# Kernel optimization log

Hardware: AMD Instinct MI355X
Metric: run time of the kernel (lower is better)

## Reference

```python
import jax, jax.numpy as jnp
import numpy as np

B, T, K, H = 8, 1024, 128, 8
TOP_K = 64
KS = 5  # conv kernel size for Q/K
DN = ('NCH', 'OIH', 'NCH')


def setup_inputs() -> dict:
    key = jax.random.key(0)
    ks = jax.random.split(key, 9)
    s = 0.05
    return {
        'x': jax.random.normal(ks[0], (B, T, K), jnp.float32),
        'Wq': jax.random.normal(ks[1], (K * H, K, KS), jnp.float32) * s,
        'bq': jax.random.normal(ks[2], (K * H,), jnp.float32) * s,
        'Wk': jax.random.normal(ks[3], (K * H, K, KS), jnp.float32) * s,
        'bk': jax.random.normal(ks[4], (K * H,), jnp.float32) * s,
        'Wv': jax.random.normal(ks[5], (K * H, K, 1), jnp.float32) * s,
        'bv': jax.random.normal(ks[6], (K * H,), jnp.float32) * s,
        'Wu': jax.random.normal(ks[7], (K, K * H), jnp.float32) * s,
        'bu': jax.random.normal(ks[8], (K,), jnp.float32) * s,
    }


def _prep(z, b, k, h, t, scale):
    # z: (b, k*h, t) conv output; torch view(b,k,h,t) then transposes -> (b,h,t,k)
    z = z.reshape(b, k, h, t)
    z = jnp.transpose(z, (0, 2, 3, 1)) * scale  # (b, h, t, k)
    # torch: transpose(1,2).contiguous().view(b*h, t, k) -- replicate exactly
    z = jnp.transpose(z, (0, 2, 1, 3)).reshape(b * h, t, k)
    return z


def reference(x, Wq, bq, Wk, bk, Wv, bv, Wu, bu):
    b, t, k = x.shape
    h = H
    xc = jnp.transpose(x, (0, 2, 1))  # (b, k, t)
    # causal left-pad KS-1 for Q/K convs; V is pointwise (kernel 1)
    q = jax.lax.conv_general_dilated(xc, Wq, (1,), [(KS - 1, 0)], dimension_numbers=DN) + bq[None, :, None]
    kk = jax.lax.conv_general_dilated(xc, Wk, (1,), [(KS - 1, 0)], dimension_numbers=DN) + bk[None, :, None]
    v = jax.lax.conv_general_dilated(xc, Wv, (1,), [(0, 0)], dimension_numbers=DN) + bv[None, :, None]
    scale = k ** -0.25
    q = _prep(q, b, k, h, t, scale)
    kk = _prep(kk, b, k, h, t, scale)
    v = _prep(v, b, k, h, t, 1.0)
    w = jnp.einsum('btk,bsk->bts', q, kk)  # (b*h, t, t)
    # top-k sparsification: keep entries >= k-th largest per row, else row min
    largest, _ = jax.lax.top_k(w, TOP_K)
    thresh = jnp.min(largest, axis=-1, keepdims=True)
    row_min = jnp.min(w, axis=-1, keepdims=True)
    w = jnp.where(w >= thresh, w, row_min)
    # causal mask (strict upper triangle -> -inf)
    causal = jnp.triu(jnp.ones((t, t), bool), 1)
    w = jnp.where(causal[None], -jnp.inf, w)
    w = jax.nn.softmax(w, axis=-1)
    out = jnp.einsum('bts,bsk->btk', w, v)  # (b*h, t, k)
    out = out.reshape(b, h, t, k)
    out = jnp.transpose(out, (0, 2, 1, 3)).reshape(b, t, k * h)
    return out @ Wu.T + bu
```

## Files before the change

kernel.cpp:

```cpp
#include <hip/hip_runtime.h>
#include <hip/hip_fp16.h>
#include <cstdint>

using f16 = _Float16;
typedef __attribute__((ext_vector_type(8))) _Float16 f16x8;
typedef __attribute__((ext_vector_type(4))) _Float16 f16x4;
typedef __attribute__((ext_vector_type(4))) float f32x4;

#define MFMA16(a, b, c) __builtin_amdgcn_mfma_f32_16x16x32_f16((a), (b), (c), 0, 0, 0)

__device__ __forceinline__ f16x8 ldfrag(const f16* p) { return *(const f16x8*)p; }

__device__ __forceinline__ void dma16(const f16* g, f16* l) {
  __builtin_amdgcn_global_load_lds(
      (const __attribute__((address_space(1))) void*)g,
      (__attribute__((address_space(3))) void*)l, 16, 0, 0);
}
__device__ __forceinline__ void wait_vm0() {
  asm volatile("s_waitcnt vmcnt(0)" ::: "memory");
}
__device__ __forceinline__ void wait_lgkm0() {
  asm volatile("s_waitcnt lgkmcnt(0)" ::: "memory");
}
__device__ __forceinline__ void wait_vm4() {
  asm volatile("s_waitcnt vmcnt(4)" ::: "memory");
}
__device__ __forceinline__ void wait_vm2() {
  asm volatile("s_waitcnt vmcnt(2)" ::: "memory");
}

static const int64_t NX = 1048576;
static const int64_t NW = 655360;
static const int64_t NV = 131072;

__global__ __launch_bounds__(256) void k0_prep(
    const float* __restrict__ x, const float* __restrict__ Wq,
    const float* __restrict__ Wk, const float* __restrict__ Wv,
    const float* __restrict__ Wu,
    f16* __restrict__ xh, f16* __restrict__ xl,
    f16* __restrict__ Wqh, f16* __restrict__ Wql,
    f16* __restrict__ Wkh, f16* __restrict__ Wkl,
    f16* __restrict__ Wvb, f16* __restrict__ Wub) {
  int64_t i = (int64_t)blockIdx.x * 256 + threadIdx.x;
  if (i < NX) {
    const float v = x[i];
    const f16 h = (f16)v;
    xh[i] = h; xl[i] = (f16)(v - (float)h);
  } else if (i < NX + NW) {
    int64_t d = i - NX;
    int j = (int)(d >> 17);
    int rem = (int)(d & 131071);
    int o = rem >> 7, c = rem & 127;
    const float v = Wq[(int64_t)(o * 128 + c) * 5 + j];
    const f16 h = (f16)v;
    Wqh[d] = h; Wql[d] = (f16)(v - (float)h);
  } else if (i < NX + 2 * NW) {
    int64_t d = i - NX - NW;
    int j = (int)(d >> 17);
    int rem = (int)(d & 131071);
    int o = rem >> 7, c = rem & 127;
    const float v = Wk[(int64_t)(o * 128 + c) * 5 + j];
    const f16 h = (f16)v;
    Wkh[d] = h; Wkl[d] = (f16)(v - (float)h);
  } else if (i < NX + 2 * NW + NV) {
    int64_t d = i - NX - 2 * NW;
    Wvb[d] = (f16)Wv[d];
  } else {
    int64_t d = i - NX - 2 * NW - NV;
    Wub[d] = (f16)Wu[d];
  }
}

#define STAGE_QK(DST, PASS, VALEXPR)                                    \
  {                                                                     \
    __syncthreads();                                                    \
    _Pragma("unroll")                                                   \
    for (int nt = 0; nt < 8; ++nt) {                                    \
      const int o = o0 + nt * 16 + lo;                                  \
      const int kcl = (o >> 3) & 63, hh = o & 7;                        \
      _Pragma("unroll")                                                 \
      for (int rtl = 0; rtl < 2; ++rtl) {                               \
        const int rt = (PASS) * 2 + rtl;                                \
        _Pragma("unroll")                                               \
        for (int r = 0; r < 4; ++r) {                                   \
          const int t2l = (rtl * 16 + quad * 4 + r) * 8 + hh;           \
          lds[t2l * 72 + kcl] = (VALEXPR);                              \
        }                                                               \
      }                                                                 \
    }                                                                   \
    __syncthreads();                                                    \
    _Pragma("unroll")                                                   \
    for (int p = 0; p < 8; ++p) {                                       \
      const int idx = p * 256 + tid;                                    \
      const int a = idx >> 3, c8 = (idx & 7) * 8;                       \
      *(f16x8*)(DST + ((int64_t)m * 1024 + t2b + (PASS) * 256 + a) * 128 + \
                half * 64 + c8) = *(const f16x8*)&lds[a * 72 + c8];     \
    }                                                                   \
  }

__global__ __launch_bounds__(256) void k1_conv(
    const f16* __restrict__ xh, const f16* __restrict__ xl,
    const f16* __restrict__ Wqh, const f16* __restrict__ Wql,
    const f16* __restrict__ Wkh, const f16* __restrict__ Wkl,
    const f16* __restrict__ Wvb,
    const float* __restrict__ bq, const float* __restrict__ bk,
    const float* __restrict__ bv,
    f16* __restrict__ q3h, f16* __restrict__ q3l,
    f16* __restrict__ k3h, f16* __restrict__ k3l,
    f16* __restrict__ v3T) {
  __shared__ f16 shm[36384];
  f16* const wbuf = shm;
  f16* const xbuf = shm + 18432;
  f16* const lds  = shm;
  const int tid = threadIdx.x;
  const int w = tid >> 6, lane = tid & 63;
  const int quad = lane >> 4, lo = lane & 15;
  const int r0 = blockIdx.x * 64;
  const int bb = r0 >> 10;
  const int m  = r0 >> 7;
  const int t2b = (r0 & 127) * 8;
  const int tloc = r0 & 1023;
  const int half = blockIdx.y;
  const int isK = blockIdx.z;
  const int o0 = half * 512 + w * 128;

  const f16* Wh = isK ? Wkh : Wqh;
  const f16* Wl = isK ? Wkl : Wql;
  const float* bias = isK ? bk : bq;

#pragma unroll
  for (int p = 0; p < 9; ++p) {
    const int u = p * 256 + tid;
    if (u < 2176) {
      const int row = u >> 5, tz = (u >> 4) & 1, c8 = (u & 15) * 8;
      int lt = tloc - 4 + row;
      if (lt < 0) lt = 0;
      const f16* src = (tz ? xl : xh) + ((int64_t)(bb * 1024 + lt)) * 128 + c8;
      *(f16x8*)&xbuf[row * 264 + tz * 128 + c8] = *(const f16x8*)src;
    }
  }
  __syncthreads();

  const int64_t wlane = (int64_t)(lane & 15) * 128 + (lane >> 4) * 8;

  if (!isK) {
    f32x4 av[4][8];
#pragma unroll
    for (int rt = 0; rt < 4; ++rt)
#pragma unroll
      for (int i = 0; i < 8; ++i)
#pragma unroll
        for (int r = 0; r < 4; ++r) av[rt][i][r] = 0.f;

#pragma unroll
    for (int g = 0; g < 4; ++g) {
#pragma unroll
      for (int s = 0; s < 2; ++s) {
        const int64_t vsrc = (int64_t)(o0 + (g * 2 + s) * 16) * 128 + wlane;
#pragma unroll
        for (int kk = 0; kk < 4; ++kk)
          dma16(Wvb + vsrc + kk * 32, wbuf + w * 4096 + s * 2048 + kk * 512);
      }
      wait_vm0();
#pragma unroll
      for (int kk = 0; kk < 4; ++kk) {
        f16x8 a[4];
#pragma unroll
        for (int rt = 0; rt < 4; ++rt)
          a[rt] = *(const f16x8*)&xbuf[(rt * 16 + lo + 4) * 264 + kk * 32 +
                                       quad * 8];
#pragma unroll
        for (int s = 0; s < 2; ++s) {
          const f16x8 bv8 = *(const f16x8*)&wbuf[w * 4096 + s * 2048 + kk * 512 +
                                                 quad * 128 + lo * 8];
#pragma unroll
          for (int rt = 0; rt < 4; ++rt)
            av[rt][g * 2 + s] = MFMA16(a[rt], bv8, av[rt][g * 2 + s]);
        }
      }
      wait_lgkm0();
    }
    __syncthreads();
#pragma unroll
    for (int pass = 0; pass < 2; ++pass) {
#pragma unroll
      for (int nt = 0; nt < 8; ++nt) {
        const int o = o0 + nt * 16 + lo;
        const float vbv = bv[o];
        const int kcl = (o >> 3) & 63, hh = o & 7;
#pragma unroll
        for (int rtl = 0; rtl < 2; ++rtl)
#pragma unroll
          for (int r = 0; r < 4; ++r) {
            const int t2l = (rtl * 16 + quad * 4 + r) * 8 + hh;
            lds[kcl * 264 + t2l] = (f16)(av[pass * 2 + rtl][nt][r] + vbv);
          }
      }
      __syncthreads();
#pragma unroll
      for (int p = 0; p < 8; ++p) {
        const int idx = p * 256 + tid;
        const int kcl = idx >> 5, t8 = (idx & 31) * 8;
        *(f16x8*)(v3T + ((int64_t)m * 128 + half * 64 + kcl) * 1024 + t2b +
                  pass * 256 + t8) = *(const f16x8*)&lds[kcl * 264 + t8];
      }
      __syncthreads();
    }
  }

  f32x4 aq[4][8];
#pragma unroll
  for (int rt = 0; rt < 4; ++rt)
#pragma unroll
    for (int i = 0; i < 8; ++i)
#pragma unroll
      for (int r = 0; r < 4; ++r) { aq[rt][i][r] = 0.f; }

  const int64_t wbase = wlane + (int64_t)o0 * 128;
#define ISSUE_HALF(J, KK, NTG, H)                                       \
  {                                                                     \
    _Pragma("unroll")                                                   \
    for (int ntl2 = 0; ntl2 < 2; ++ntl2) {                              \
      const int ntl_ = (H) * 2 + ntl2;                                  \
      const int64_t o_ = wbase + (int64_t)(J) * 131072 + (KK) * 32 +    \
                         (int64_t)(((NTG) * 4 + ntl_) * 16) * 128;      \
      dma16(Wh + o_, wbuf + w * 4096 + ntl_ * 1024);                    \
      dma16(Wl + o_, wbuf + w * 4096 + ntl_ * 1024 + 512);              \
    }                                                                   \
  }

  ISSUE_HALF(0, 0, 0, 0)
  ISSUE_HALF(0, 0, 0, 1)

  const bool z0 = (tloc == 0);
  for (int j = 0; j < 5; ++j) {
    f16x8 ah[4], al[4];
#pragma unroll
    for (int c = 0; c < 8; ++c) {
      const int kk = c >> 1, ntg = c & 1;
      if (ntg == 0) {
#pragma unroll
        for (int rt = 0; rt < 4; ++rt) {
          ah[rt] = *(const f16x8*)&xbuf[(rt * 16 + lo + j) * 264 + kk * 32 +
                                        quad * 8];
          al[rt] = *(const f16x8*)&xbuf[(rt * 16 + lo + j) * 264 + 128 +
                                        kk * 32 + quad * 8];
        }
        if (z0 && (lo + j < 4)) {
#pragma unroll
          for (int e = 0; e < 8; ++e) { ah[0][e] = (f16)0; al[0][e] = (f16)0; }
        }
      }
      const int nj = (c == 7) ? j + 1 : j;
      const int nkk = (c == 7) ? 0 : ((c + 1) >> 1);
      const int nntg = (c == 7) ? 0 : ((c + 1) & 1);
      const bool more = (c < 7) || (j < 4);

      wait_vm4();
#pragma unroll
      for (int ntl = 0; ntl < 2; ++ntl) {
        const int nt = ntg * 4 + ntl;
        const f16x8 bh = *(const f16x8*)&wbuf[w * 4096 + ntl * 1024 +
                                              quad * 128 + lo * 8];
        const f16x8 bl = *(const f16x8*)&wbuf[w * 4096 + ntl * 1024 + 512 +
                                              quad * 128 + lo * 8];
#pragma unroll
        for (int rt = 0; rt < 4; ++rt) {
          aq[rt][nt] = MFMA16(ah[rt], bh, aq[rt][nt]);
          aq[rt][nt] = MFMA16(ah[rt], bl, aq[rt][nt]);
          aq[rt][nt] = MFMA16(al[rt], bh, aq[rt][nt]);
        }
      }
      wait_lgkm0();
      if (more) ISSUE_HALF(nj, nkk, nntg, 0)

      if (c == 7) {
        if (j == 4) wait_vm0(); else wait_vm4();
      } else {
        wait_vm4();
      }
#pragma unroll
      for (int ntl = 2; ntl < 4; ++ntl) {
        const int nt = ntg * 4 + ntl;
        const f16x8 bh = *(const f16x8*)&wbuf[w * 4096 + ntl * 1024 +
                                              quad * 128 + lo * 8];
        const f16x8 bl = *(const f16x8*)&wbuf[w * 4096 + ntl * 1024 + 512 +
                                              quad * 128 + lo * 8];
#pragma unroll
        for (int rt = 0; rt < 4; ++rt) {
          aq[rt][nt] = MFMA16(ah[rt], bh, aq[rt][nt]);
          aq[rt][nt] = MFMA16(ah[rt], bl, aq[rt][nt]);
          aq[rt][nt] = MFMA16(al[rt], bh, aq[rt][nt]);
        }
      }
      wait_lgkm0();
      if (more) ISSUE_HALF(nj, nkk, nntg, 1)
    }
  }
#undef ISSUE_HALF

  const float SC = 0.29730177875068026f;
#pragma unroll
  for (int nt = 0; nt < 8; ++nt) {
    const int o = o0 + nt * 16 + lo;
    const float vb = bias[o];
#pragma unroll
    for (int rt = 0; rt < 4; ++rt)
#pragma unroll
      for (int r = 0; r < 4; ++r) aq[rt][nt][r] = (aq[rt][nt][r] + vb) * SC;
  }

  if (!isK) {
    STAGE_QK(q3h, 0, (f16)aq[rt][nt][r])
    STAGE_QK(q3h, 1, (f16)aq[rt][nt][r])
    STAGE_QK(q3l, 0, (f16)(aq[rt][nt][r] - (float)(f16)aq[rt][nt][r]))
    STAGE_QK(q3l, 1, (f16)(aq[rt][nt][r] - (float)(f16)aq[rt][nt][r]))
  } else {
    STAGE_QK(k3h, 0, (f16)aq[rt][nt][r])
    STAGE_QK(k3h, 1, (f16)aq[rt][nt][r])
    STAGE_QK(k3l, 0, (f16)(aq[rt][nt][r] - (float)(f16)aq[rt][nt][r]))
    STAGE_QK(k3l, 1, (f16)(aq[rt][nt][r] - (float)(f16)aq[rt][nt][r]))
  }
}

__global__ __launch_bounds__(512, 4) void k234_attn(
    const f16* __restrict__ q3h, const f16* __restrict__ q3l,
    const f16* __restrict__ k3h, const f16* __restrict__ k3l,
    const f16* __restrict__ v3T, f16* __restrict__ A) {
  __shared__ __align__(16) char smem[70144];
  float* const SbQ = (float*)smem;
  f16* const PbufA = (f16*)smem;
  f16* const PbufB = (f16*)(smem + 16640);
  f16* const kbuf = (f16*)(smem + 33280);
  f16* const qlds = (f16*)(smem + 66048);
  const int tid = threadIdx.x;
  const int w = tid >> 6, lane = tid & 63;
  const int quad = lane >> 4, lo = lane & 15;
  const int qd = lane & 3, cit = lane >> 2;
  const int qsw = qd ^ ((cit >> 1) & 3);
  const int fro = (lo * 4 + (quad ^ ((lo >> 1) & 3))) * 8;
  const int hid = blockIdx.y * 32 + blockIdx.x;
  const int m = (hid & 7) * 8 + ((hid >> 3) >> 5);
  const int r0 = ((hid >> 3) & 31) * 32;

  unsigned key[2][2][16];
  unsigned kmn[2][2];
#pragma unroll
  for (int g = 0; g < 2; ++g)
#pragma unroll
    for (int rr = 0; rr < 2; ++rr) kmn[g][rr] = 0xFFFFFFFFu;

#pragma unroll
  for (int half = 0; half < 2; ++half) {
    f32x4 acc[2][4];
#pragma unroll
    for (int g = 0; g < 2; ++g)
#pragma unroll
      for (int i = 0; i < 4; ++i)
#pragma unroll
        for (int r = 0; r < 4; ++r) acc[g][i][r] = 0.f;

    for (int kp = 0; kp < 2; ++kp) {
#pragma unroll
      for (int kkh = 0; kkh < 2; ++kkh) {
        __syncthreads();
        if (w < 4) {
          const int h_ = w & 1, grp_ = w >> 1;
          const f16* qsrc = (h_ ? q3l : q3h) +
              ((int64_t)m * 1024 + r0 + grp_ * 16 + lo) * 128 +
              (kp * 2 + kkh) * 32 + quad * 8;
          dma16(qsrc, qlds + w * 512);
        }
        wait_vm0();
        __syncthreads();

#define KISS(CC, PAIR)                                                   \
  {                                                                      \
    const int64_t rowg =                                                 \
        (int64_t)(m * 1024 + half * 512 + (CC) * 128 + w * 16 + cit) *   \
            128 + (kp * 2 + kkh) * 32 + qsw * 8;                         \
    dma16(k3h + rowg, kbuf + (w * 4 + (PAIR) * 2) * 512);                \
    dma16(k3l + rowg, kbuf + (w * 4 + (PAIR) * 2 + 1) * 512);            \
  }
        KISS(0, 0)
        KISS(1, 1)
#pragma unroll
        for (int cc = 0; cc < 4; ++cc) {
          if (cc < 3) wait_vm2();
          else wait_vm0();
          const int pair = cc & 1;
          const f16x8 qh0 = ldfrag(qlds + 0 * 512 + lane * 8);
          const f16x8 ql0 = ldfrag(qlds + 1 * 512 + lane * 8);
          const f16x8 qh1 = ldfrag(qlds + 2 * 512 + lane * 8);
          const f16x8 ql1 = ldfrag(qlds + 3 * 512 + lane * 8);
          const f16x8 bh =
              *(const f16x8*)(kbuf + (w * 4 + pair * 2) * 512 + fro);
          const f16x8 bl =
              *(const f16x8*)(kbuf + (w * 4 + pair * 2 + 1) * 512 + fro);
          acc[0][cc] = MFMA16(qh0, bh, acc[0][cc]);
          acc[0][cc] = MFMA16(qh0, bl, acc[0][cc]);
          acc[0][cc] = MFMA16(ql0, bh, acc[0][cc]);
          acc[1][cc] = MFMA16(qh1, bh, acc[1][cc]);
          acc[1][cc] = MFMA16(qh1, bl, acc[1][cc]);
          acc[1][cc] = MFMA16(ql1, bh, acc[1][cc]);
          wait_lgkm0();
          if (cc == 0) KISS(2, 0)
          if (cc == 1) KISS(3, 1)
        }
#undef KISS
      }
    }

#pragma unroll
    for (int grp = 0; grp < 2; ++grp) {
#pragma unroll
      for (int q = 0; q < 2; ++q) {
#pragma unroll
        for (int c2 = 0; c2 < 2; ++c2)
#pragma unroll
          for (int r = 0; r < 4; ++r)
            SbQ[(quad * 4 + r) * 268 + c2 * 128 + w * 16 + lo] =
                acc[grp][q * 2 + c2][r];
        __syncthreads();
#pragma unroll
        for (int rr = 0; rr < 2; ++rr) {
          const float4 f4 =
              *(const float4*)(SbQ + (w * 2 + rr) * 268 + lane * 4);
          const float fe[4] = {f4.x, f4.y, f4.z, f4.w};
#pragma unroll
          for (int e = 0; e < 4; ++e) {
            const unsigned u = __builtin_bit_cast(unsigned, fe[e]);
            const unsigned k = (u & 0x80000000u) ? ~u : (u | 0x80000000u);
            key[grp][rr][half * 8 + q * 4 + e] = k;
            kmn[grp][rr] = min(kmn[grp][rr], k);
          }
        }
        __syncthreads();
      }
    }
  }

  const int64_t vrow = (int64_t)(m * 128 + w * 16 + cit) * 1024;
  const int nkbM = ((r0 + 16) >> 6) + 1;
#define VISSUE(KB, PAIR)                                                 \
  {                                                                      \
    dma16(v3T + vrow + (KB) * 64 + qsw * 8,                              \
          kbuf + (w * 4 + (PAIR) * 2) * 512);                            \
    dma16(v3T + vrow + (KB) * 64 + 32 + qsw * 8,                         \
          kbuf + (w * 4 + (PAIR) * 2 + 1) * 512);                       \
  }
  VISSUE(0, 0)
  if (nkbM > 1) VISSUE(1, 1)

#pragma unroll
  for (int off = 32; off; off >>= 1) {
#pragma unroll
    for (int g = 0; g < 2; ++g)
#pragma unroll
      for (int rr = 0; rr < 2; ++rr)
        kmn[g][rr] = min(kmn[g][rr],
                         (unsigned)__shfl_xor((int)kmn[g][rr], off));
  }
  unsigned th[2][2] = {{0u, 0u}, {0u, 0u}};
  {
    bool dn[2][2] = {{false, false}, {false, false}};
    for (int b = 31; b >= 0; --b) {
      bool all = true;
#pragma unroll
      for (int g = 0; g < 2; ++g)
#pragma unroll
        for (int rr = 0; rr < 2; ++rr) {
          if (!dn[g][rr]) {
            const unsigned c = th[g][rr] | (1u << b);
            int cnt = 0;
#pragma unroll
            for (int i = 0; i < 16; ++i)
              cnt += (int)__popcll(__ballot(key[g][rr][i] >= c));
            if (cnt >= 64) { th[g][rr] = c; if (cnt == 64) dn[g][rr] = true; }
          }
          all = all && dn[g][rr];
        }
      if (all) break;
    }
  }

  float ev[2][2][16];
  float inv[2][2];
#pragma unroll
  for (int g = 0; g < 2; ++g)
#pragma unroll
    for (int rr = 0; rr < 2; ++rr) {
      const unsigned kth = th[g][rr];
      const unsigned kmv = kmn[g][rr];
      const int t2 = r0 + g * 16 + w * 2 + rr;
      const unsigned umn = (kmv & 0x80000000u) ? (kmv ^ 0x80000000u) : ~kmv;
      const float mn = __builtin_bit_cast(float, umn);
      const unsigned ukv = (kth & 0x80000000u) ? (kth ^ 0x80000000u) : ~kth;
      const float kv = __builtin_bit_cast(float, ukv);
      float sum = 0.f;
#pragma unroll
      for (int j = 0; j < 16; ++j) {
        const int s = (j >> 2) * 256 + lane * 4 + (j & 3);
        const unsigned k = key[g][rr][j];
        const unsigned uu = (k & 0x80000000u) ? (k ^ 0x80000000u) : ~k;
        const float f = __builtin_bit_cast(float, uu);
        const float ww = (k >= kth) ? f : mn;
        const float x = (s <= t2) ? __expf(ww - kv) : 0.f;
        ev[g][rr][j] = x;
        sum += x;
      }
      for (int off = 32; off; off >>= 1) sum += __shfl_xor(sum, off);
      inv[g][rr] = 1.0f / sum;
    }

  {
    const int nkb0h = nkbM < 8 ? nkbM : 8;
#pragma unroll
    for (int g = 0; g < 2; ++g) {
      f16* const pb = g ? PbufB : PbufA;
#pragma unroll
      for (int rr = 0; rr < 2; ++rr) {
        f16* prow = pb + (w * 2 + rr) * 520;
#pragma unroll
        for (int i2 = 0; i2 < 2; ++i2) {
          f16x4 pk;
#pragma unroll
          for (int e = 0; e < 4; ++e)
            pk[e] = (f16)(ev[g][rr][i2 * 4 + e] * inv[g][rr]);
          *(f16x4*)(prow + i2 * 256 + lane * 4) = pk;
        }
      }
    }
    __syncthreads();

    f32x4 oaA0, oaA1, oaB0, oaB1;
#pragma unroll
    for (int r = 0; r < 4; ++r) {
      oaA0[r] = 0.f; oaA1[r] = 0.f; oaB0[r] = 0.f; oaB1[r] = 0.f;
    }
    for (int kb = 0; kb < nkb0h; ++kb) {
      if (kb + 1 < nkb0h) wait_vm2();
      else wait_vm0();
      const int pair = kb & 1;
      {
        const f16x8 vf0 =
            *(const f16x8*)(kbuf + (w * 4 + pair * 2) * 512 + fro);
        const f16x8 vf1 =
            *(const f16x8*)(kbuf + (w * 4 + pair * 2 + 1) * 512 + fro);
        const f16x8 aA0 =
            *(const f16x8*)(PbufA + lo * 520 + kb * 64 + quad * 8);
        const f16x8 aA1 =
            *(const f16x8*)(PbufA + lo * 520 + kb * 64 + 32 + quad * 8);
        const f16x8 aB0 =
            *(const f16x8*)(PbufB + lo * 520 + kb * 64 + quad * 8);
        const f16x8 aB1 =
            *(const f16x8*)(PbufB + lo * 520 + kb * 64 + 32 + quad * 8);
        oaA0 = MFMA16(aA0, vf0, oaA0);
        oaA1 = MFMA16(aA1, vf1, oaA1);
        oaB0 = MFMA16(aB0, vf0, oaB0);
        oaB1 = MFMA16(aB1, vf1, oaB1);
      }
      wait_lgkm0();
      if (kb + 2 < nkb0h) VISSUE(kb + 2, pair)
    }

    if (nkbM > 8) {
      VISSUE(8, 0)
      if (nkbM > 9) VISSUE(9, 1)
      __syncthreads();
#pragma unroll
      for (int g = 0; g < 2; ++g) {
        f16* const pb = g ? PbufB : PbufA;
#pragma unroll
        for (int rr = 0; rr < 2; ++rr) {
          f16* prow = pb + (w * 2 + rr) * 520;
#pragma unroll
          for (int i2 = 0; i2 < 2; ++i2) {
            f16x4 pk;
#pragma unroll
            for (int e = 0; e < 4; ++e)
              pk[e] = (f16)(ev[g][rr][8 + i2 * 4 + e] * inv[g][rr]);
            *(f16x4*)(prow + i2 * 256 + lane * 4) = pk;
          }
        }
      }
      __syncthreads();
      for (int kb = 8; kb < nkbM; ++kb) {
        if (kb + 1 < nkbM) wait_vm2();
        else wait_vm0();
        const int pair = kb & 1;
        {
          const f16x8 vf0 =
              *(const f16x8*)(kbuf + (w * 4 + pair * 2) * 512 + fro);
          const f16x8 vf1 =
              *(const f16x8*)(kbuf + (w * 4 + pair * 2 + 1) * 512 + fro);
          const f16x8 aA0 =
              *(const f16x8*)(PbufA + lo * 520 + (kb - 8) * 64 + quad * 8);
          const f16x8 aA1 =
              *(const f16x8*)(PbufA + lo * 520 + (kb - 8) * 64 + 32 + quad * 8);
          const f16x8 aB0 =
              *(const f16x8*)(PbufB + lo * 520 + (kb - 8) * 64 + quad * 8);
          const f16x8 aB1 =
              *(const f16x8*)(PbufB + lo * 520 + (kb - 8) * 64 + 32 + quad * 8);
          oaA0 = MFMA16(aA0, vf0, oaA0);
          oaA1 = MFMA16(aA1, vf1, oaA1);
          oaB0 = MFMA16(aB0, vf0, oaB0);
          oaB1 = MFMA16(aB1, vf1, oaB1);
        }
        wait_lgkm0();
        if (kb + 2 < nkbM) VISSUE(kb + 2, pair)
      }
    }

#pragma unroll
    for (int r = 0; r < 4; ++r) {
      A[((int64_t)m * 1024 + r0 + quad * 4 + r) * 128 + w * 16 + lo] =
          (f16)(oaA0[r] + oaA1[r]);
      A[((int64_t)m * 1024 + r0 + 16 + quad * 4 + r) * 128 + w * 16 + lo] =
          (f16)(oaB0[r] + oaB1[r]);
    }
  }
#undef VISSUE
}

__global__ __launch_bounds__(256) void k5_proj(
    const f16* __restrict__ A, const f16* __restrict__ Wub,
    const float* __restrict__ bu, float* __restrict__ out) {
  const int w = threadIdx.x >> 6, lane = threadIdx.x & 63;
  const int quad = lane >> 4, lo = lane & 15;
  const int rt = w & 1, ch = w >> 1;
  const int r0 = blockIdx.x * 32 + rt * 16;
  const int r = r0 + lo;
  const int bI = r >> 10, t2 = r & 1023;

  f32x4 acc[4];
#pragma unroll
  for (int i = 0; i < 4; ++i)
#pragma unroll
    for (int rr = 0; rr < 4; ++rr) acc[i][rr] = 0.f;

#pragma unroll 2
  for (int kk = 0; kk < 32; ++kk) {
    const int o = kk * 32 + quad * 8;
    const int j = o >> 7, kc = o & 127;
    f16x8 a = ldfrag(A + (((int64_t)(bI * 8 + j) * 1024 + t2) * 128 + kc));
    f16x8 wb[4];
#pragma unroll
    for (int nt = 0; nt < 4; ++nt)
      wb[nt] = ldfrag(Wub + (int64_t)(ch * 64 + nt * 16 + lo) * 1024 + o);
#pragma unroll
    for (int nt = 0; nt < 4; ++nt) acc[nt] = MFMA16(a, wb[nt], acc[nt]);
  }
#pragma unroll
  for (int nt = 0; nt < 4; ++nt) {
    const int col = ch * 64 + nt * 16 + lo;
    const float bias = bu[col];
#pragma unroll
    for (int rr = 0; rr < 4; ++rr) {
      const int row = r0 + quad * 4 + rr;
      out[(int64_t)row * 128 + col] = acc[nt][rr] + bias;
    }
  }
}

extern "C" void kernel_launch(void* const* d_in, const int* in_sizes, int n_in,
                              void* d_out, int out_size, void* d_ws, size_t ws_size,
                              hipStream_t stream) {
  const float* x  = (const float*)d_in[0];
  const float* Wq = (const float*)d_in[1];
  const float* bq = (const float*)d_in[2];
  const float* Wk = (const float*)d_in[3];
  const float* bk = (const float*)d_in[4];
  const float* Wv = (const float*)d_in[5];
  const float* bv = (const float*)d_in[6];
  const float* Wu = (const float*)d_in[7];
  const float* bu = (const float*)d_in[8];
  float* out = (float*)d_out;

  char* ws = (char*)d_ws;
  f16* xh  = (f16*)ws;  ws += 2097152;
  f16* xl  = (f16*)ws;  ws += 2097152;
  f16* Wqh = (f16*)ws;  ws += 1310720;
  f16* Wql = (f16*)ws;  ws += 1310720;
  f16* Wkh = (f16*)ws;  ws += 1310720;
  f16* Wkl = (f16*)ws;  ws += 1310720;
  f16* Wvb = (f16*)ws;  ws += 262144;
  f16* Wub = (f16*)ws;  ws += 262144;
  f16* q3h = (f16*)ws;  ws += 16777216;
  f16* q3l = (f16*)ws;  ws += 16777216;
  f16* k3h = (f16*)ws;  ws += 16777216;
  f16* k3l = (f16*)ws;  ws += 16777216;
  f16* v3T = (f16*)ws;  ws += 16777216;
  f16* A   = (f16*)ws;  ws += 16777216;

  k0_prep<<<10240, 256, 0, stream>>>(x, Wq, Wk, Wv, Wu,
                                     xh, xl, Wqh, Wql, Wkh, Wkl, Wvb, Wub);

  k1_conv<<<dim3(128, 2, 2), 256, 0, stream>>>(xh, xl, Wqh, Wql, Wkh, Wkl, Wvb,
                                               bq, bk, bv, q3h, q3l, k3h, k3l,
                                               v3T);

  k234_attn<<<dim3(32, 64), 512, 0, stream>>>(q3h, q3l, k3h, k3l, v3T, A);

  k5_proj<<<256, 256, 0, stream>>>(A, Wub, bu, out);

  (void)in_sizes; (void)n_in; (void)out_size; (void)ws_size;
}
```

Baseline: 383.3 us.

## Preload full Q tile once and run continuous K prefetch pipeline across halves

Q's high and low fragments for all four 32-wide k-segments are loaded into LDS once before the score loop. This replaces the per-segment Q reload that needed two block barriers each time. The K double-buffer prefetch now runs as one flat 32-step pipeline, so the next loads are issued across segment and half boundaries instead of draining at each one. The LDS layout is reshuffled so the Q buffer aliases PbufB, which reduces shared memory. The cost is that the aliasing must not overlap Q with the SbQ scratch written between the halves.

```diff
diff --git a/kernel.cpp b/kernel.cpp
--- a/kernel.cpp
+++ b/kernel.cpp
@@ -327,12 +327,12 @@
     const f16* __restrict__ q3h, const f16* __restrict__ q3l,
     const f16* __restrict__ k3h, const f16* __restrict__ k3l,
     const f16* __restrict__ v3T, f16* __restrict__ A) {
-  __shared__ __align__(16) char smem[70144];
+  __shared__ __align__(16) char smem[66560];
   float* const SbQ = (float*)smem;
   f16* const PbufA = (f16*)smem;
-  f16* const PbufB = (f16*)(smem + 16640);
-  f16* const kbuf = (f16*)(smem + 33280);
-  f16* const qlds = (f16*)(smem + 66048);
+  f16* const qlds = (f16*)(smem + 17152);
+  f16* const PbufB = (f16*)(smem + 17152);
+  f16* const kbuf = (f16*)(smem + 33792);
   const int tid = threadIdx.x;
   const int w = tid >> 6, lane = tid & 63;
   const int quad = lane >> 4, lo = lane & 15;
@@ -350,6 +350,31 @@
 #pragma unroll
     for (int rr = 0; rr < 2; ++rr) kmn[g][rr] = 0xFFFFFFFFu;
 
+  {
+#pragma unroll
+    for (int s2 = 0; s2 < 2; ++s2) {
+      const int sl = w * 2 + s2;
+      const int seg = sl >> 2, grp_ = (sl >> 1) & 1, h_ = sl & 1;
+      const f16* qsrc = (h_ ? q3l : q3h) +
+          ((int64_t)m * 1024 + r0 + grp_ * 16 + lo) * 128 + seg * 32 +
+          quad * 8;
+      dma16(qsrc, qlds + sl * 512);
+    }
+    wait_vm0();
+    __syncthreads();
+  }
+
+#define KISS(HALF, C, PAIR)                                              \
+  {                                                                      \
+    const int64_t rowg =                                                 \
+        (int64_t)(m * 1024 + (HALF) * 512 + ((C) & 3) * 128 + w * 16 +   \
+                  cit) * 128 + ((C) >> 2) * 32 + qsw * 8;                \
+    dma16(k3h + rowg, kbuf + (w * 4 + (PAIR) * 2) * 512);                \
+    dma16(k3l + rowg, kbuf + (w * 4 + (PAIR) * 2 + 1) * 512);            \
+  }
+
+  KISS(0, 0, 0)
+  KISS(0, 1, 1)
 #pragma unroll
   for (int half = 0; half < 2; ++half) {
     f32x4 acc[2][4];
@@ -360,55 +385,29 @@
 #pragma unroll
         for (int r = 0; r < 4; ++r) acc[g][i][r] = 0.f;
 
-    for (int kp = 0; kp < 2; ++kp) {
-#pragma unroll
-      for (int kkh = 0; kkh < 2; ++kkh) {
-        __syncthreads();
-        if (w < 4) {
-          const int h_ = w & 1, grp_ = w >> 1;
-          const f16* qsrc = (h_ ? q3l : q3h) +
-              ((int64_t)m * 1024 + r0 + grp_ * 16 + lo) * 128 +
-              (kp * 2 + kkh) * 32 + quad * 8;
-          dma16(qsrc, qlds + w * 512);
-        }
-        wait_vm0();
-        __syncthreads();
-
-#define KISS(CC, PAIR)                                                   \
-  {                                                                      \
-    const int64_t rowg =                                                 \
-        (int64_t)(m * 1024 + half * 512 + (CC) * 128 + w * 16 + cit) *   \
-            128 + (kp * 2 + kkh) * 32 + qsw * 8;                         \
-    dma16(k3h + rowg, kbuf + (w * 4 + (PAIR) * 2) * 512);                \
-    dma16(k3l + rowg, kbuf + (w * 4 + (PAIR) * 2 + 1) * 512);            \
-  }
-        KISS(0, 0)
-        KISS(1, 1)
-#pragma unroll
-        for (int cc = 0; cc < 4; ++cc) {
-          if (cc < 3) wait_vm2();
-          else wait_vm0();
-          const int pair = cc & 1;
-          const f16x8 qh0 = ldfrag(qlds + 0 * 512 + lane * 8);
-          const f16x8 ql0 = ldfrag(qlds + 1 * 512 + lane * 8);
-          const f16x8 qh1 = ldfrag(qlds + 2 * 512 + lane * 8);
-          const f16x8 ql1 = ldfrag(qlds + 3 * 512 + lane * 8);
-          const f16x8 bh =
-              *(const f16x8*)(kbuf + (w * 4 + pair * 2) * 512 + fro);
-          const f16x8 bl =
-              *(const f16x8*)(kbuf + (w * 4 + pair * 2 + 1) * 512 + fro);
-          acc[0][cc] = MFMA16(qh0, bh, acc[0][cc]);
-          acc[0][cc] = MFMA16(qh0, bl, acc[0][cc]);
-          acc[0][cc] = MFMA16(ql0, bh, acc[0][cc]);
-          acc[1][cc] = MFMA16(qh1, bh, acc[1][cc]);
-          acc[1][cc] = MFMA16(qh1, bl, acc[1][cc]);
-          acc[1][cc] = MFMA16(ql1, bh, acc[1][cc]);
-          wait_lgkm0();
-          if (cc == 0) KISS(2, 0)
-          if (cc == 1) KISS(3, 1)
-        }
-#undef KISS
-      }
+#pragma unroll
+    for (int c = 0; c < 16; ++c) {
+      const int g = half * 16 + c;
+      if (g == 31) wait_vm0();
+      else wait_vm2();
+      const int pair = c & 1;
+      const int seg = c >> 2, cc = c & 3;
+      const f16x8 qh0 = ldfrag(qlds + (seg * 4 + 0) * 512 + lane * 8);
+      const f16x8 ql0 = ldfrag(qlds + (seg * 4 + 1) * 512 + lane * 8);
+      const f16x8 qh1 = ldfrag(qlds + (seg * 4 + 2) * 512 + lane * 8);
+      const f16x8 ql1 = ldfrag(qlds + (seg * 4 + 3) * 512 + lane * 8);
+      const f16x8 bh = *(const f16x8*)(kbuf + (w * 4 + pair * 2) * 512 + fro);
+      const f16x8 bl =
+          *(const f16x8*)(kbuf + (w * 4 + pair * 2 + 1) * 512 + fro);
+      acc[0][cc] = MFMA16(qh0, bh, acc[0][cc]);
+      acc[0][cc] = MFMA16(qh0, bl, acc[0][cc]);
+      acc[0][cc] = MFMA16(ql0, bh, acc[0][cc]);
+      acc[1][cc] = MFMA16(qh1, bh, acc[1][cc]);
+      acc[1][cc] = MFMA16(qh1, bl, acc[1][cc]);
+      acc[1][cc] = MFMA16(ql1, bh, acc[1][cc]);
+      wait_lgkm0();
+      const int gn = g + 2;
+      if (gn < 32) KISS(gn >> 4, gn & 15, gn & 1)
     }
 
 #pragma unroll
@@ -439,6 +438,7 @@
       }
     }
   }
+#undef KISS
 
   const int64_t vrow = (int64_t)(m * 128 + w * 16 + cit) * 1024;
   const int nkbM = ((r0 + 16) >> 6) + 1;
```

New measurement: 374.7 us. 2.2% less time.
